# Performance work log

Hardware: AMD Instinct MI355X
Metric: run time of the kernel (lower is better)

The kernel has to match this reference:

```python
import jax, jax.numpy as jnp
import numpy as np

B, C, O, K, H, W = 32, 256, 256, 7, 31, 31


def _unfold(x, k):
    """Extract kxk sliding windows (stride 1, no padding, no dilation).

    x: [B, C, H, W] -> patches [B, C, k, k, Ho, Wo]
    """
    _, _, h, w = x.shape
    ho, wo = h - k + 1, w - k + 1
    # fixed small loop over k*k window offsets (k=7 -> 49 cheap slices)
    rows = []
    for i in range(k):
        cols = [x[:, :, i:i + ho, j:j + wo] for j in range(k)]
        rows.append(jnp.stack(cols, axis=2))  # [B, C, k, Ho, Wo]
    return jnp.stack(rows, axis=2)  # [B, C, k, k, Ho, Wo]


def setup_inputs() -> dict:
    key = jax.random.key(0)
    k1, k2, k3, k4 = jax.random.split(key, 4)
    x = jax.random.normal(k1, (B, C, H, W), dtype=jnp.float32)
    kernel = jax.random.normal(k2, (B, C, K, K), dtype=jnp.float32)
    weight = jax.random.normal(k3, (O, C, K, K), dtype=jnp.float32) * 0.02
    bias = jax.random.normal(k4, (O,), dtype=jnp.float32) * 0.02
    return {"x": x, "kernel": kernel, "weight": weight, "bias": bias}


def reference(x, kernel, weight, bias):
    k = weight.shape[-1]
    patches = _unfold(x, k)  # [B, C, k, k, Ho, Wo]
    # fused: (patches * kernel[..., None, None]) contracted with weight
    # torch: einsum('ijklmn,ojkl->iomn', patches * kernel_view, weight)
    out = jnp.einsum('bcklhw,bckl,ockl->bohw', patches, kernel, weight)
    out = out + bias[None, :, None, None]
    return out
```

## Files before the change

### kernel.cpp

```cpp
#include <hip/hip_runtime.h>
#include <hip/hip_bf16.h>

typedef __attribute__((ext_vector_type(8)))  short short8;
typedef __attribute__((ext_vector_type(4)))  float floatx4;
typedef __attribute__((ext_vector_type(16))) float floatx16;

#define BB 32
#define CC 256
#define OO 256
#define KS 7
#define HH 31
#define WW 31
#define HO 25
#define PP 625
#define SS 49

#define SLAB_PITCH 40
#define SLAB_ROWS  310

#define WT4_ELEMS  ((size_t)SS * 8 * 2 * CC * 16)
#define WT4_BYTES  (WT4_ELEMS * 2)
#define KERNF_BYTES ((size_t)BB * SS * CC * 4)
#define WMOD_ELEMS ((size_t)BB * WT4_ELEMS)
#define WMOD_BYTES (WMOD_ELEMS * 2)

static __device__ __forceinline__ unsigned pk2(float lo, float hi) {
    float2 f; f.x = lo; f.y = hi;
    __hip_bfloat162 h = __float22bfloat162_rn(f);
    unsigned r;
    __builtin_memcpy(&r, &h, sizeof(r));
    return r;
}
static __device__ __forceinline__ float bflo(unsigned u) {
    return __builtin_bit_cast(float, u << 16);
}
static __device__ __forceinline__ float bfhi(unsigned u) {
    return __builtin_bit_cast(float, u & 0xffff0000u);
}

static __device__ __forceinline__ uint4 modpack(uint4 wv, float4 k0, float4 k1) {
    float p0 = bflo(wv.x) * k0.x, p1 = bfhi(wv.x) * k0.y;
    float p2 = bflo(wv.y) * k0.z, p3 = bfhi(wv.y) * k0.w;
    float p4 = bflo(wv.z) * k1.x, p5 = bfhi(wv.z) * k1.y;
    float p6 = bflo(wv.w) * k1.z, p7 = bfhi(wv.w) * k1.w;
    uint4 r;
    r.x = pk2(p0, p1); r.y = pk2(p2, p3); r.z = pk2(p4, p5); r.w = pk2(p6, p7);
    return r;
}

__global__ __launch_bounds__(256) void repack_w(const float* __restrict__ w,
                                                unsigned short* __restrict__ wt4) {
    const int bid = blockIdx.x;
    const int s = bid >> 3, cb = bid & 7;
    const int o = threadIdx.x;
    const float* src = w + ((size_t)o * CC + cb * 32) * SS + s;
    float v[32];
#pragma unroll
    for (int ci = 0; ci < 32; ++ci) v[ci] = src[(size_t)ci * SS];
#pragma unroll
    for (int kh = 0; kh < 2; ++kh) {
        unsigned short* dst = wt4 + ((size_t)bid * 2 + kh) * (CC * 16) + o * 16;
        uint4 p0, p1;
        p0.x = pk2(v[kh*16+0], v[kh*16+1]);  p0.y = pk2(v[kh*16+2], v[kh*16+3]);
        p0.z = pk2(v[kh*16+4], v[kh*16+5]);  p0.w = pk2(v[kh*16+6], v[kh*16+7]);
        p1.x = pk2(v[kh*16+8], v[kh*16+9]);  p1.y = pk2(v[kh*16+10], v[kh*16+11]);
        p1.z = pk2(v[kh*16+12], v[kh*16+13]); p1.w = pk2(v[kh*16+14], v[kh*16+15]);
        *(uint4*)(dst)     = p0;
        *(uint4*)(dst + 8) = p1;
    }
}

__global__ __launch_bounds__(256) void repack_k(const float* __restrict__ kern,
                                                float* __restrict__ kernf) {
    const int bid = blockIdx.x;
    const int b = bid / KS, kk = bid % KS;
    const int c = threadIdx.x;
    const float* src = kern + ((size_t)b * CC + c) * SS + kk * KS;
#pragma unroll
    for (int ll = 0; ll < KS; ++ll)
        kernf[((size_t)b * SS + kk * KS + ll) * CC + c] = src[ll];
}

__global__ __launch_bounds__(256) void premod(
        const unsigned short* __restrict__ wt4, const float* __restrict__ kern,
        unsigned short* __restrict__ wmod) {
    const int bid = blockIdx.x;
    const int b = bid / 392, rc = bid % 392;
    const int s = rc >> 3, cb = rc & 7;
    const int o = threadIdx.x;
    const float* kp = kern + ((size_t)b * CC + cb * 32) * SS + s;
    float kf[32];
#pragma unroll
    for (int ci = 0; ci < 32; ++ci) kf[ci] = kp[(size_t)ci * SS];
#pragma unroll
    for (int kh = 0; kh < 2; ++kh) {
        const size_t off = ((size_t)rc * 2 + kh) * (CC * 16) + o * 16;
        uint4 w0 = *(const uint4*)(wt4 + off);
        uint4 w1 = *(const uint4*)(wt4 + off + 8);
        float4 k0a, k0b, k1a, k1b;
        k0a.x = kf[kh*16+0];  k0a.y = kf[kh*16+1];  k0a.z = kf[kh*16+2];  k0a.w = kf[kh*16+3];
        k0b.x = kf[kh*16+4];  k0b.y = kf[kh*16+5];  k0b.z = kf[kh*16+6];  k0b.w = kf[kh*16+7];
        k1a.x = kf[kh*16+8];  k1a.y = kf[kh*16+9];  k1a.z = kf[kh*16+10]; k1a.w = kf[kh*16+11];
        k1b.x = kf[kh*16+12]; k1b.y = kf[kh*16+13]; k1b.z = kf[kh*16+14]; k1b.w = kf[kh*16+15];
        uint4 m0 = modpack(w0, k0a, k0b);
        uint4 m1 = modpack(w1, k1a, k1b);
        unsigned short* dst = wmod + (size_t)b * WT4_ELEMS + off;
        *(uint4*)(dst)     = m0;
        *(uint4*)(dst + 8) = m1;
    }
}

__global__ __launch_bounds__(256, 4) void dwconv_big(
        const float* __restrict__ x, const unsigned short* __restrict__ wmod,
        const float* __restrict__ bias, float* __restrict__ out) {
    __shared__ unsigned short slab[SLAB_ROWS * SLAB_PITCH];

    const int tid = threadIdx.x;
    const int id = blockIdx.x;
    const int hi = id / 80, rem = id % 80;
    const int px = rem >> 3;
    const int g = hi * 8 + (rem & 7);
    const int b = g >> 2, oy = g & 3;

    const int p0 = px * 64, o0 = oy * 64;
    const int h0 = p0 / HO;
    const int pmax = (p0 + 63 < PP - 1) ? p0 + 63 : PP - 1;
    const int rows = pmax / HO - h0 + 7;
    const int npos = rows * WW;

    const int lane = tid & 63, kw = tid >> 6;
    const int l32 = lane & 31, half = lane >> 5;

    int bOff[2];
#pragma unroll
    for (int ph = 0; ph < 2; ++ph) {
        int p = p0 + ph * 32 + l32;
        if (p > PP - 1) p = PP - 1;
        int h = p / HO, ww_ = p - h * HO;
        bOff[ph] = ((h - h0) * WW + ww_) * SLAB_PITCH + half * 8;
    }

    const int s0 = kw * 12 + (kw > 0 ? 1 : 0);
    const int ns = kw ? 12 : 13;

    const unsigned short* wmodb = wmod + (size_t)b * WT4_ELEMS
                                  + (size_t)(o0 + l32) * 16 + half * 8;

    floatx16 acc[2][2];
#pragma unroll
    for (int oh = 0; oh < 2; ++oh)
#pragma unroll
        for (int ph = 0; ph < 2; ++ph)
#pragma unroll
            for (int r = 0; r < 16; ++r) acc[oh][ph][r] = 0.f;

    for (int cb = 0; cb < 8; ++cb) {
        __syncthreads();
        {
            const float* xsrc = x + ((size_t)(b * CC + cb * 32 + kw * 8)) * (HH * WW)
                                  + h0 * WW;
#pragma unroll
            for (int it = 0; it < 5; ++it) {
                int pos = lane + it * 64;
                if (pos < npos) {
                    float v[8];
#pragma unroll
                    for (int j = 0; j < 8; ++j) v[j] = xsrc[j * (HH * WW) + pos];
                    uint4 pkt;
                    pkt.x = pk2(v[0], v[1]); pkt.y = pk2(v[2], v[3]);
                    pkt.z = pk2(v[4], v[5]); pkt.w = pk2(v[6], v[7]);
                    *(uint4*)(slab + pos * SLAB_PITCH + kw * 8) = pkt;
                }
            }
        }
        __syncthreads();

        const unsigned short* aptr = wmodb + (size_t)(s0 * 8 + cb) * 8192;

        uint4 wa0 = *(const uint4*)(aptr);
        uint4 wa1 = *(const uint4*)(aptr + 512);
        uint4 wa2 = *(const uint4*)(aptr + 4096);
        uint4 wa3 = *(const uint4*)(aptr + 4096 + 512);

        int s = s0, kk = s0 / KS, ll = s0 - (s0 / KS) * KS;
        for (int si = 0; si < ns; ++si) {
            uint4 wn0, wn1, wn2, wn3;
            if (si + 1 < ns) {
                aptr += 65536;
                wn0 = *(const uint4*)(aptr);
                wn1 = *(const uint4*)(aptr + 512);
                wn2 = *(const uint4*)(aptr + 4096);
                wn3 = *(const uint4*)(aptr + 4096 + 512);
            } else {
                wn0 = wa0; wn1 = wa1; wn2 = wa2; wn3 = wa3;
            }

            const unsigned short* slabS = slab + (kk * WW + ll) * SLAB_PITCH;
            short8 sb00 = *(const short8*)(slabS + bOff[0]);
            short8 sb01 = *(const short8*)(slabS + bOff[0] + 16);
            short8 sb10 = *(const short8*)(slabS + bOff[1]);
            short8 sb11 = *(const short8*)(slabS + bOff[1] + 16);

            short8 a00 = __builtin_bit_cast(short8, wa0);
            short8 a10 = __builtin_bit_cast(short8, wa1);
            short8 a01 = __builtin_bit_cast(short8, wa2);
            short8 a11 = __builtin_bit_cast(short8, wa3);

            acc[0][0] = __builtin_amdgcn_mfma_f32_32x32x16_bf16(a00, sb00, acc[0][0], 0, 0, 0);
            acc[0][1] = __builtin_amdgcn_mfma_f32_32x32x16_bf16(a00, sb10, acc[0][1], 0, 0, 0);
            acc[1][0] = __builtin_amdgcn_mfma_f32_32x32x16_bf16(a10, sb00, acc[1][0], 0, 0, 0);
            acc[1][1] = __builtin_amdgcn_mfma_f32_32x32x16_bf16(a10, sb10, acc[1][1], 0, 0, 0);
            acc[0][0] = __builtin_amdgcn_mfma_f32_32x32x16_bf16(a01, sb01, acc[0][0], 0, 0, 0);
            acc[0][1] = __builtin_amdgcn_mfma_f32_32x32x16_bf16(a01, sb11, acc[0][1], 0, 0, 0);
            acc[1][0] = __builtin_amdgcn_mfma_f32_32x32x16_bf16(a11, sb01, acc[1][0], 0, 0, 0);
            acc[1][1] = __builtin_amdgcn_mfma_f32_32x32x16_bf16(a11, sb11, acc[1][1], 0, 0, 0);

            wa0 = wn0; wa1 = wn1; wa2 = wn2; wa3 = wn3;
            ++s; if (++ll == KS) { ll = 0; ++kk; }
        }
    }

    float* red = (float*)slab;
    __syncthreads();
    if (kw == 3) {
#pragma unroll
        for (int oh = 0; oh < 2; ++oh)
#pragma unroll
            for (int ph = 0; ph < 2; ++ph)
#pragma unroll
                for (int c = 0; c < 4; ++c) {
                    floatx4 v4 = {acc[oh][ph][4*c+0], acc[oh][ph][4*c+1],
                                  acc[oh][ph][4*c+2], acc[oh][ph][4*c+3]};
                    *(floatx4*)(red + (ph * 32 + l32) * 68 + oh * 32 + c * 8 + 4 * half) = v4;
                }
    }
    __syncthreads();
    if (kw == 2) {
#pragma unroll
        for (int oh = 0; oh < 2; ++oh)
#pragma unroll
            for (int ph = 0; ph < 2; ++ph)
#pragma unroll
                for (int c = 0; c < 4; ++c) {
                    float* rp = red + (ph * 32 + l32) * 68 + oh * 32 + c * 8 + 4 * half;
                    floatx4 v4 = *(floatx4*)rp;
                    v4[0] += acc[oh][ph][4*c+0]; v4[1] += acc[oh][ph][4*c+1];
                    v4[2] += acc[oh][ph][4*c+2]; v4[3] += acc[oh][ph][4*c+3];
                    *(floatx4*)rp = v4;
                }
    }
    __syncthreads();
    if (kw == 1) {
#pragma unroll
        for (int oh = 0; oh < 2; ++oh)
#pragma unroll
            for (int ph = 0; ph < 2; ++ph)
#pragma unroll
                for (int c = 0; c < 4; ++c) {
                    float* rp = red + (ph * 32 + l32) * 68 + oh * 32 + c * 8 + 4 * half;
                    floatx4 v4 = *(floatx4*)rp;
                    v4[0] += acc[oh][ph][4*c+0]; v4[1] += acc[oh][ph][4*c+1];
                    v4[2] += acc[oh][ph][4*c+2]; v4[3] += acc[oh][ph][4*c+3];
                    *(floatx4*)rp = v4;
                }
    }
    __syncthreads();
    if (kw == 0) {
#pragma unroll
        for (int oh = 0; oh < 2; ++oh)
#pragma unroll
            for (int c = 0; c < 4; ++c) {
                const int ob = o0 + oh * 32 + c * 8 + 4 * half;
                const float4 bv = *(const float4*)(bias + ob);
#pragma unroll
                for (int ph = 0; ph < 2; ++ph) {
                    const int p = p0 + ph * 32 + l32;
                    floatx4 v4 = *(floatx4*)(red + (ph * 32 + l32) * 68 + oh * 32 + c * 8 + 4 * half);
                    if (p < PP) {
                        out[((size_t)(b * OO + ob + 0)) * PP + p] = v4[0] + acc[oh][ph][4*c+0] + bv.x;
                        out[((size_t)(b * OO + ob + 1)) * PP + p] = v4[1] + acc[oh][ph][4*c+1] + bv.y;
                        out[((size_t)(b * OO + ob + 2)) * PP + p] = v4[2] + acc[oh][ph][4*c+2] + bv.z;
                        out[((size_t)(b * OO + ob + 3)) * PP + p] = v4[3] + acc[oh][ph][4*c+3] + bv.w;
                    }
                }
            }
    }
}

#define SLAB2_ROWS 372
__global__ __launch_bounds__(256, 3) void dwconv_mid(
        const float* __restrict__ x,
        const unsigned short* __restrict__ wt4, const float* __restrict__ kernf,
        const float* __restrict__ bias, float* __restrict__ out) {
    __shared__ unsigned short slab[SLAB2_ROWS * SLAB_PITCH];

    const int tid = threadIdx.x;
    const int id = blockIdx.x;
    const int oy = id & 3;
    const int t  = id >> 2;
    const int px = t % 5, b = t / 5;
    const int p0 = px * 128, o0 = oy * 64;
    const int h0 = p0 / HO;
    const int rows = (HH - h0) < 12 ? (HH - h0) : 12;
    const int npos = rows * WW;

    const int lane = tid & 63, wid = tid >> 6;
    const int pw = wid & 1, kw = wid >> 1;
    const int lo16 = lane & 15, quad = lane >> 4;

    int bOff[4];
#pragma unroll
    for (int pt = 0; pt < 4; ++pt) {
        int p = p0 + pw * 64 + pt * 16 + lo16;
        if (p > PP - 1) p = PP - 1;
        int h = p / HO, ww_ = p - h * HO;
        bOff[pt] = ((h - h0) * WW + ww_) * SLAB_PITCH + quad * 8;
    }

    const int s0 = kw ? 25 : 0;
    const int ns = kw ? 24 : 25;

    floatx4 acc[4][4];
#pragma unroll
    for (int at = 0; at < 4; ++at)
#pragma unroll
        for (int pt = 0; pt < 4; ++pt)
            acc[at][pt] = (floatx4){0.f, 0.f, 0.f, 0.f};

    for (int cb = 0; cb < 8; ++cb) {
        __syncthreads();
        {
            const int coct = wid;
            const float* xsrc = x + ((size_t)(b * CC + cb * 32 + coct * 8)) * (HH * WW)
                                  + h0 * WW;
#pragma unroll
            for (int it = 0; it < 6; ++it) {
                int pos = lane + it * 64;
                if (pos < npos) {
                    float v[8];
#pragma unroll
                    for (int j = 0; j < 8; ++j) v[j] = xsrc[j * (HH * WW) + pos];
                    uint4 pkt;
                    pkt.x = pk2(v[0], v[1]); pkt.y = pk2(v[2], v[3]);
                    pkt.z = pk2(v[4], v[5]); pkt.w = pk2(v[6], v[7]);
                    *(uint4*)(slab + pos * SLAB_PITCH + coct * 8) = pkt;
                }
            }
        }
        __syncthreads();

        const unsigned short* aptrA = wt4 +
            ((size_t)(s0 * 8 + cb) * 2 + (quad >> 1)) * 4096 +
            (size_t)(o0 + lo16) * 16 + (quad & 1) * 8;
        const float* kptr = kernf + ((size_t)b * SS + s0) * CC + cb * 32 + quad * 8;

        uint4 wa[4];
        wa[0] = *(const uint4*)(aptrA);
        wa[1] = *(const uint4*)(aptrA + 256);
        wa[2] = *(const uint4*)(aptrA + 512);
        wa[3] = *(const uint4*)(aptrA + 768);
        float4 kq0 = *(const float4*)(kptr);
        float4 kq1 = *(const float4*)(kptr + 4);

        for (int si = 0; si < ns; ++si) {
            const int s = s0 + si;
            uint4 wn[4]; float4 kn0, kn1;
            if (si + 1 < ns) {
                aptrA += 65536;
                kptr  += CC;
                wn[0] = *(const uint4*)(aptrA);
                wn[1] = *(const uint4*)(aptrA + 256);
                wn[2] = *(const uint4*)(aptrA + 512);
                wn[3] = *(const uint4*)(aptrA + 768);
                kn0 = *(const float4*)(kptr);
                kn1 = *(const float4*)(kptr + 4);
            } else {
                wn[0] = wa[0]; wn[1] = wa[1]; wn[2] = wa[2]; wn[3] = wa[3];
                kn0 = kq0; kn1 = kq1;
            }

            const int kk = s / KS, ll = s - kk * KS;
            const unsigned short* slabS = slab + (kk * WW + ll) * SLAB_PITCH;

            short8 sb0 = *(const short8*)(slabS + bOff[0]);
            short8 sb1 = *(const short8*)(slabS + bOff[1]);
            short8 sb2 = *(const short8*)(slabS + bOff[2]);
            short8 sb3 = *(const short8*)(slabS + bOff[3]);

            short8 sa0 = __builtin_bit_cast(short8, modpack(wa[0], kq0, kq1));
            short8 sa1 = __builtin_bit_cast(short8, modpack(wa[1], kq0, kq1));
            short8 sa2 = __builtin_bit_cast(short8, modpack(wa[2], kq0, kq1));
            short8 sa3 = __builtin_bit_cast(short8, modpack(wa[3], kq0, kq1));

            acc[0][0] = __builtin_amdgcn_mfma_f32_16x16x32_bf16(sa0, sb0, acc[0][0], 0, 0, 0);
            acc[0][1] = __builtin_amdgcn_mfma_f32_16x16x32_bf16(sa0, sb1, acc[0][1], 0, 0, 0);
            acc[0][2] = __builtin_amdgcn_mfma_f32_16x16x32_bf16(sa0, sb2, acc[0][2], 0, 0, 0);
            acc[0][3] = __builtin_amdgcn_mfma_f32_16x16x32_bf16(sa0, sb3, acc[0][3], 0, 0, 0);
            acc[1][0] = __builtin_amdgcn_mfma_f32_16x16x32_bf16(sa1, sb0, acc[1][0], 0, 0, 0);
            acc[1][1] = __builtin_amdgcn_mfma_f32_16x16x32_bf16(sa1, sb1, acc[1][1], 0, 0, 0);
            acc[1][2] = __builtin_amdgcn_mfma_f32_16x16x32_bf16(sa1, sb2, acc[1][2], 0, 0, 0);
            acc[1][3] = __builtin_amdgcn_mfma_f32_16x16x32_bf16(sa1, sb3, acc[1][3], 0, 0, 0);
            acc[2][0] = __builtin_amdgcn_mfma_f32_16x16x32_bf16(sa2, sb0, acc[2][0], 0, 0, 0);
            acc[2][1] = __builtin_amdgcn_mfma_f32_16x16x32_bf16(sa2, sb1, acc[2][1], 0, 0, 0);
            acc[2][2] = __builtin_amdgcn_mfma_f32_16x16x32_bf16(sa2, sb2, acc[2][2], 0, 0, 0);
            acc[2][3] = __builtin_amdgcn_mfma_f32_16x16x32_bf16(sa2, sb3, acc[2][3], 0, 0, 0);
            acc[3][0] = __builtin_amdgcn_mfma_f32_16x16x32_bf16(sa3, sb0, acc[3][0], 0, 0, 0);
            acc[3][1] = __builtin_amdgcn_mfma_f32_16x16x32_bf16(sa3, sb1, acc[3][1], 0, 0, 0);
            acc[3][2] = __builtin_amdgcn_mfma_f32_16x16x32_bf16(sa3, sb2, acc[3][2], 0, 0, 0);
            acc[3][3] = __builtin_amdgcn_mfma_f32_16x16x32_bf16(sa3, sb3, acc[3][3], 0, 0, 0);

            wa[0] = wn[0]; wa[1] = wn[1]; wa[2] = wn[2]; wa[3] = wn[3];
            kq0 = kn0; kq1 = kn1;
        }
    }

    float* red = (float*)slab;
    for (int round = 0; round < 2; ++round) {
        __syncthreads();
        if (kw == 1 && pw == round) {
#pragma unroll
            for (int at = 0; at < 4; ++at)
#pragma unroll
                for (int pt = 0; pt < 4; ++pt)
                    *(floatx4*)(red + (pt * 16 + lo16) * 68 + at * 16 + quad * 4)
                        = acc[at][pt];
        }
        __syncthreads();
        if (kw == 0 && pw == round) {
#pragma unroll
            for (int at = 0; at < 4; ++at) {
                const float4 bv = *(const float4*)(bias + o0 + at * 16 + quad * 4);
#pragma unroll
                for (int pt = 0; pt < 4; ++pt) {
                    floatx4 v = *(const floatx4*)(red + (pt * 16 + lo16) * 68
                                                  + at * 16 + quad * 4);
                    int p = p0 + round * 64 + pt * 16 + lo16;
                    if (p < PP) {
                        const int ob = o0 + at * 16 + quad * 4;
                        out[((size_t)(b * OO + ob + 0)) * PP + p] = acc[at][pt][0] + v[0] + bv.x;
                        out[((size_t)(b * OO + ob + 1)) * PP + p] = acc[at][pt][1] + v[1] + bv.y;
                        out[((size_t)(b * OO + ob + 2)) * PP + p] = acc[at][pt][2] + v[2] + bv.z;
                        out[((size_t)(b * OO + ob + 3)) * PP + p] = acc[at][pt][3] + v[3] + bv.w;
                    }
                }
            }
        }
    }
}

__global__ __launch_bounds__(256) void dwconv_naive(
        const float* __restrict__ x, const float* __restrict__ kern,
        const float* __restrict__ w, const float* __restrict__ bias,
        float* __restrict__ out) {
    const int idx = blockIdx.x * 256 + threadIdx.x;
    if (idx >= BB * OO * PP) return;
    const int p = idx % PP;
    const int o = (idx / PP) % OO;
    const int b = idx / (PP * OO);
    const int h = p / HO;
    const int wq = p - h * HO;
    float acc = 0.f;
    for (int c = 0; c < CC; ++c) {
        const float* xp = x + ((size_t)(b * CC + c)) * (HH * WW) + h * WW + wq;
        const float* kp = kern + ((size_t)b * CC + c) * SS;
        const float* wp = w + ((size_t)o * CC + c) * SS;
#pragma unroll
        for (int s = 0; s < SS; ++s) {
            const int kk = s / KS;
            const int ll = s - kk * KS;
            acc += xp[kk * WW + ll] * kp[s] * wp[s];
        }
    }
    out[idx] = acc + bias[o];
}

extern "C" void kernel_launch(void* const* d_in, const int* in_sizes, int n_in,
                              void* d_out, int out_size, void* d_ws, size_t ws_size,
                              hipStream_t stream) {
    const float* x    = (const float*)d_in[0];
    const float* kern = (const float*)d_in[1];
    const float* w    = (const float*)d_in[2];
    const float* bias = (const float*)d_in[3];
    float* out = (float*)d_out;

    if (ws_size >= WT4_BYTES + WMOD_BYTES) {
        unsigned short* wt4  = (unsigned short*)d_ws;
        unsigned short* wmod = (unsigned short*)((char*)d_ws + WT4_BYTES);
        repack_w<<<dim3(SS * 8), dim3(256), 0, stream>>>(w, wt4);
        premod<<<dim3(BB * SS * 8), dim3(256), 0, stream>>>(wt4, kern, wmod);
        dwconv_big<<<dim3(1280), dim3(256), 0, stream>>>(x, wmod, bias, out);
    } else if (ws_size >= WT4_BYTES + KERNF_BYTES) {
        unsigned short* wt4 = (unsigned short*)d_ws;
        float* kernf = (float*)((char*)d_ws + WT4_BYTES);
        repack_w<<<dim3(SS * 8), dim3(256), 0, stream>>>(w, wt4);
        repack_k<<<dim3(BB * KS), dim3(256), 0, stream>>>(kern, kernf);
        dwconv_mid<<<dim3(640), dim3(256), 0, stream>>>(x, wt4, kernf, bias, out);
    } else {
        const int total = BB * OO * PP;
        dwconv_naive<<<dim3((total + 255) / 256), dim3(256), 0, stream>>>(
            x, kern, w, bias, out);
    }
}
```

Measured before the change: 307.8 us.

## Double pixel tile per block in dwconv_big to reuse modulated weights

Measured after the change: 340.5 us. +10.6%, slower.

```diff
diff --git a/kernel.cpp b/kernel.cpp
--- a/kernel.cpp
+++ b/kernel.cpp
@@ -16,7 +16,7 @@
 #define SS 49
 
 #define SLAB_PITCH 40
-#define SLAB_ROWS  310
+#define SLAB_ROWS  372
 
 #define WT4_ELEMS  ((size_t)SS * 8 * 2 * CC * 16)
 #define WT4_BYTES  (WT4_ELEMS * 2)
@@ -110,30 +110,30 @@
     }
 }
 
-__global__ __launch_bounds__(256, 4) void dwconv_big(
+__global__ __launch_bounds__(256, 2) void dwconv_big(
         const float* __restrict__ x, const unsigned short* __restrict__ wmod,
         const float* __restrict__ bias, float* __restrict__ out) {
     __shared__ unsigned short slab[SLAB_ROWS * SLAB_PITCH];
 
     const int tid = threadIdx.x;
     const int id = blockIdx.x;
-    const int hi = id / 80, rem = id % 80;
+    const int hi = id / 40, rem = id % 40;
     const int px = rem >> 3;
     const int g = hi * 8 + (rem & 7);
     const int b = g >> 2, oy = g & 3;
 
-    const int p0 = px * 64, o0 = oy * 64;
+    const int p0 = px * 128, o0 = oy * 64;
     const int h0 = p0 / HO;
-    const int pmax = (p0 + 63 < PP - 1) ? p0 + 63 : PP - 1;
+    const int pmax = (p0 + 127 < PP - 1) ? p0 + 127 : PP - 1;
     const int rows = pmax / HO - h0 + 7;
     const int npos = rows * WW;
 
     const int lane = tid & 63, kw = tid >> 6;
     const int l32 = lane & 31, half = lane >> 5;
 
-    int bOff[2];
-#pragma unroll
-    for (int ph = 0; ph < 2; ++ph) {
+    int bOff[4];
+#pragma unroll
+    for (int ph = 0; ph < 4; ++ph) {
         int p = p0 + ph * 32 + l32;
         if (p > PP - 1) p = PP - 1;
         int h = p / HO, ww_ = p - h * HO;
@@ -146,11 +146,11 @@
     const unsigned short* wmodb = wmod + (size_t)b * WT4_ELEMS
                                   + (size_t)(o0 + l32) * 16 + half * 8;
 
-    floatx16 acc[2][2];
+    floatx16 acc[2][4];
 #pragma unroll
     for (int oh = 0; oh < 2; ++oh)
 #pragma unroll
-        for (int ph = 0; ph < 2; ++ph)
+        for (int ph = 0; ph < 4; ++ph)
 #pragma unroll
             for (int r = 0; r < 16; ++r) acc[oh][ph][r] = 0.f;
 
@@ -160,7 +160,7 @@
             const float* xsrc = x + ((size_t)(b * CC + cb * 32 + kw * 8)) * (HH * WW)
                                   + h0 * WW;
 #pragma unroll
-            for (int it = 0; it < 5; ++it) {
+            for (int it = 0; it < 6; ++it) {
                 int pos = lane + it * 64;
                 if (pos < npos) {
                     float v[8];
@@ -182,7 +182,7 @@
         uint4 wa2 = *(const uint4*)(aptr + 4096);
         uint4 wa3 = *(const uint4*)(aptr + 4096 + 512);
 
-        int s = s0, kk = s0 / KS, ll = s0 - (s0 / KS) * KS;
+        int kk = s0 / KS, ll = s0 - (s0 / KS) * KS;
         for (int si = 0; si < ns; ++si) {
             uint4 wn0, wn1, wn2, wn3;
             if (si + 1 < ns) {
@@ -196,103 +196,105 @@
             }
 
             const unsigned short* slabS = slab + (kk * WW + ll) * SLAB_PITCH;
-            short8 sb00 = *(const short8*)(slabS + bOff[0]);
-            short8 sb01 = *(const short8*)(slabS + bOff[0] + 16);
-            short8 sb10 = *(const short8*)(slabS + bOff[1]);
-            short8 sb11 = *(const short8*)(slabS + bOff[1] + 16);
-
             short8 a00 = __builtin_bit_cast(short8, wa0);
             short8 a10 = __builtin_bit_cast(short8, wa1);
             short8 a01 = __builtin_bit_cast(short8, wa2);
             short8 a11 = __builtin_bit_cast(short8, wa3);
 
-            acc[0][0] = __builtin_amdgcn_mfma_f32_32x32x16_bf16(a00, sb00, acc[0][0], 0, 0, 0);
-            acc[0][1] = __builtin_amdgcn_mfma_f32_32x32x16_bf16(a00, sb10, acc[0][1], 0, 0, 0);
-            acc[1][0] = __builtin_amdgcn_mfma_f32_32x32x16_bf16(a10, sb00, acc[1][0], 0, 0, 0);
-            acc[1][1] = __builtin_amdgcn_mfma_f32_32x32x16_bf16(a10, sb10, acc[1][1], 0, 0, 0);
-            acc[0][0] = __builtin_amdgcn_mfma_f32_32x32x16_bf16(a01, sb01, acc[0][0], 0, 0, 0);
-            acc[0][1] = __builtin_amdgcn_mfma_f32_32x32x16_bf16(a01, sb11, acc[0][1], 0, 0, 0);
-            acc[1][0] = __builtin_amdgcn_mfma_f32_32x32x16_bf16(a11, sb01, acc[1][0], 0, 0, 0);
-            acc[1][1] = __builtin_amdgcn_mfma_f32_32x32x16_bf16(a11, sb11, acc[1][1], 0, 0, 0);
+#pragma unroll
+            for (int ph = 0; ph < 4; ++ph) {
+                short8 sbk0 = *(const short8*)(slabS + bOff[ph]);
+                short8 sbk1 = *(const short8*)(slabS + bOff[ph] + 16);
+                acc[0][ph] = __builtin_amdgcn_mfma_f32_32x32x16_bf16(a00, sbk0, acc[0][ph], 0, 0, 0);
+                acc[1][ph] = __builtin_amdgcn_mfma_f32_32x32x16_bf16(a10, sbk0, acc[1][ph], 0, 0, 0);
+                acc[0][ph] = __builtin_amdgcn_mfma_f32_32x32x16_bf16(a01, sbk1, acc[0][ph], 0, 0, 0);
+                acc[1][ph] = __builtin_amdgcn_mfma_f32_32x32x16_bf16(a11, sbk1, acc[1][ph], 0, 0, 0);
+            }
 
             wa0 = wn0; wa1 = wn1; wa2 = wn2; wa3 = wn3;
-            ++s; if (++ll == KS) { ll = 0; ++kk; }
+            if (++ll == KS) { ll = 0; ++kk; }
         }
     }
 
     float* red = (float*)slab;
-    __syncthreads();
-    if (kw == 3) {
-#pragma unroll
-        for (int oh = 0; oh < 2; ++oh)
-#pragma unroll
-            for (int ph = 0; ph < 2; ++ph)
+#pragma unroll
+    for (int round = 0; round < 2; ++round) {
+        __syncthreads();
+        if (kw == 3) {
+#pragma unroll
+            for (int oh = 0; oh < 2; ++oh)
+#pragma unroll
+                for (int phl = 0; phl < 2; ++phl)
+#pragma unroll
+                    for (int c = 0; c < 4; ++c) {
+                        const int ph = round * 2 + phl;
+                        floatx4 v4 = {acc[oh][ph][4*c+0], acc[oh][ph][4*c+1],
+                                      acc[oh][ph][4*c+2], acc[oh][ph][4*c+3]};
+                        *(floatx4*)(red + (phl * 32 + l32) * 68 + oh * 32 + c * 8 + 4 * half) = v4;
+                    }
+        }
+        __syncthreads();
+        if (kw == 2) {
+#pragma unroll
+            for (int oh = 0; oh < 2; ++oh)
+#pragma unroll
+                for (int phl = 0; phl < 2; ++phl)
+#pragma unroll
+                    for (int c = 0; c < 4; ++c) {
+                        const int ph = round * 2 + phl;
+                        float* rp = red + (phl * 32 + l32) * 68 + oh * 32 + c * 8 + 4 * half;
+                        floatx4 v4 = *(floatx4*)rp;
+                        v4[0] += acc[oh][ph][4*c+0]; v4[1] += acc[oh][ph][4*c+1];
+                        v4[2] += acc[oh][ph][4*c+2]; v4[3] += acc[oh][ph][4*c+3];
+                        *(floatx4*)rp = v4;
+                    }
+        }
+        __syncthreads();
+        if (kw == 1) {
+#pragma unroll
+            for (int oh = 0; oh < 2; ++oh)
+#pragma unroll
+                for (int phl = 0; phl < 2; ++phl)
+#pragma unroll
+                    for (int c = 0; c < 4; ++c) {
+                        const int ph = round * 2 + phl;
+                        float* rp = red + (phl * 32 + l32) * 68 + oh * 32 + c * 8 + 4 * half;
+                        floatx4 v4 = *(floatx4*)rp;
+                        v4[0] += acc[oh][ph][4*c+0]; v4[1] += acc[oh][ph][4*c+1];
+                        v4[2] += acc[oh][ph][4*c+2]; v4[3] += acc[oh][ph][4*c+3];
+                        *(floatx4*)rp = v4;
+                    }
+        }
+        __syncthreads();
+        if (kw == 0) {
+#pragma unroll
+            for (int oh = 0; oh < 2; ++oh)
 #pragma unroll
                 for (int c = 0; c < 4; ++c) {
-                    floatx4 v4 = {acc[oh][ph][4*c+0], acc[oh][ph][4*c+1],
-                                  acc[oh][ph][4*c+2], acc[oh][ph][4*c+3]};
-                    *(floatx4*)(red + (ph * 32 + l32) * 68 + oh * 32 + c * 8 + 4 * half) = v4;
-                }
-    }
-    __syncthreads();
-    if (kw == 2) {
-#pragma unroll
-        for (int oh = 0; oh < 2; ++oh)
-#pragma unroll
-            for (int ph = 0; ph < 2; ++ph)
-#pragma unroll
-                for (int c = 0; c < 4; ++c) {
-                    float* rp = red + (ph * 32 + l32) * 68 + oh * 32 + c * 8 + 4 * half;
-                    floatx4 v4 = *(floatx4*)rp;
-                    v4[0] += acc[oh][ph][4*c+0]; v4[1] += acc[oh][ph][4*c+1];
-                    v4[2] += acc[oh][ph][4*c+2]; v4[3] += acc[oh][ph][4*c+3];
-                    *(floatx4*)rp = v4;
-                }
-    }
-    __syncthreads();
-    if (kw == 1) {
-#pragma unroll
-        for (int oh = 0; oh < 2; ++oh)
-#pragma unroll
-            for (int ph = 0; ph < 2; ++ph)
-#pragma unroll
-                for (int c = 0; c < 4; ++c) {
-                    float* rp = red + (ph * 32 + l32) * 68 + oh * 32 + c * 8 + 4 * half;
-                    floatx4 v4 = *(floatx4*)rp;
-                    v4[0] += acc[oh][ph][4*c+0]; v4[1] += acc[oh][ph][4*c+1];
-                    v4[2] += acc[oh][ph][4*c+2]; v4[3] += acc[oh][ph][4*c+3];
-                    *(floatx4*)rp = v4;
-                }
-    }
-    __syncthreads();
-    if (kw == 0) {
-#pragma unroll
-        for (int oh = 0; oh < 2; ++oh)
-#pragma unroll
-            for (int c = 0; c < 4; ++c) {
-                const int ob = o0 + oh * 32 + c * 8 + 4 * half;
-                const float4 bv = *(const float4*)(bias + ob);
-#pragma unroll
-                for (int ph = 0; ph < 2; ++ph) {
-                    const int p = p0 + ph * 32 + l32;
-                    floatx4 v4 = *(floatx4*)(red + (ph * 32 + l32) * 68 + oh * 32 + c * 8 + 4 * half);
-                    if (p < PP) {
-                        out[((size_t)(b * OO + ob + 0)) * PP + p] = v4[0] + acc[oh][ph][4*c+0] + bv.x;
-                        out[((size_t)(b * OO + ob + 1)) * PP + p] = v4[1] + acc[oh][ph][4*c+1] + bv.y;
-                        out[((size_t)(b * OO + ob + 2)) * PP + p] = v4[2] + acc[oh][ph][4*c+2] + bv.z;
-                        out[((size_t)(b * OO + ob + 3)) * PP + p] = v4[3] + acc[oh][ph][4*c+3] + bv.w;
+                    const int ob = o0 + oh * 32 + c * 8 + 4 * half;
+                    const float4 bv = *(const float4*)(bias + ob);
+#pragma unroll
+                    for (int phl = 0; phl < 2; ++phl) {
+                        const int ph = round * 2 + phl;
+                        const int p = p0 + ph * 32 + l32;
+                        floatx4 v4 = *(floatx4*)(red + (phl * 32 + l32) * 68 + oh * 32 + c * 8 + 4 * half);
+                        if (p < PP) {
+                            out[((size_t)(b * OO + ob + 0)) * PP + p] = v4[0] + acc[oh][ph][4*c+0] + bv.x;
+                            out[((size_t)(b * OO + ob + 1)) * PP + p] = v4[1] + acc[oh][ph][4*c+1] + bv.y;
+                            out[((size_t)(b * OO + ob + 2)) * PP + p] = v4[2] + acc[oh][ph][4*c+2] + bv.z;
+                            out[((size_t)(b * OO + ob + 3)) * PP + p] = v4[3] + acc[oh][ph][4*c+3] + bv.w;
+                        }
                     }
                 }
-            }
-    }
-}
-
-#define SLAB2_ROWS 372
+        }
+    }
+}
+
 __global__ __launch_bounds__(256, 3) void dwconv_mid(
         const float* __restrict__ x,
         const unsigned short* __restrict__ wt4, const float* __restrict__ kernf,
         const float* __restrict__ bias, float* __restrict__ out) {
-    __shared__ unsigned short slab[SLAB2_ROWS * SLAB_PITCH];
+    __shared__ unsigned short slab[SLAB_ROWS * SLAB_PITCH];
 
     const int tid = threadIdx.x;
     const int id = blockIdx.x;
@@ -488,7 +490,7 @@
         unsigned short* wmod = (unsigned short*)((char*)d_ws + WT4_BYTES);
         repack_w<<<dim3(SS * 8), dim3(256), 0, stream>>>(w, wt4);
         premod<<<dim3(BB * SS * 8), dim3(256), 0, stream>>>(wt4, kern, wmod);
-        dwconv_big<<<dim3(1280), dim3(256), 0, stream>>>(x, wmod, bias, out);
+        dwconv_big<<<dim3(640), dim3(256), 0, stream>>>(x, wmod, bias, out);
     } else if (ws_size >= WT4_BYTES + KERNF_BYTES) {
         unsigned short* wt4 = (unsigned short*)d_ws;
         float* kernf = (float*)((char*)d_ws + WT4_BYTES);
```

## Pre-convert x to padded bf16 slabs and load them into LDS directly

Applied to the files above, without the earlier changes.

Result: slower. 351.2 us (+14.1%).

```diff
diff --git a/kernel.cpp b/kernel.cpp
--- a/kernel.cpp
+++ b/kernel.cpp
@@ -15,14 +15,17 @@
 #define PP 625
 #define SS 49
 
-#define SLAB_PITCH 40
-#define SLAB_ROWS  310
+#define PITCH 40
 
 #define WT4_ELEMS  ((size_t)SS * 8 * 2 * CC * 16)
 #define WT4_BYTES  (WT4_ELEMS * 2)
 #define KERNF_BYTES ((size_t)BB * SS * CC * 4)
 #define WMOD_ELEMS ((size_t)BB * WT4_ELEMS)
 #define WMOD_BYTES (WMOD_ELEMS * 2)
+
+#define XSLICE_E   38440
+#define XSLICE_B   76880
+#define XBF_BYTES  ((size_t)BB * 8 * XSLICE_B + 2048)
 
 static __device__ __forceinline__ unsigned pk2(float lo, float hi) {
     float2 f; f.x = lo; f.y = hi;
@@ -36,6 +39,12 @@
 }
 static __device__ __forceinline__ float bfhi(unsigned u) {
     return __builtin_bit_cast(float, u & 0xffff0000u);
+}
+
+static __device__ __forceinline__ void gload_lds16(const void* g, void* l) {
+    __builtin_amdgcn_global_load_lds(
+        (const __attribute__((address_space(1))) unsigned int*)g,
+        (__attribute__((address_space(3))) unsigned int*)l, 16, 0, 0);
 }
 
 static __device__ __forceinline__ uint4 modpack(uint4 wv, float4 k0, float4 k1) {
@@ -110,10 +119,23 @@
     }
 }
 
-__global__ __launch_bounds__(256, 4) void dwconv_big(
-        const float* __restrict__ x, const unsigned short* __restrict__ wmod,
+__global__ __launch_bounds__(256) void xbf_prep(const float* __restrict__ x,
+                                                unsigned short* __restrict__ xbf) {
+    const int bid = blockIdx.x;
+    const int b = bid >> 3, cb = bid & 7;
+    const int ci = threadIdx.x & 31, pg = threadIdx.x >> 5;
+    const float* src = x + ((size_t)(b * CC + cb * 32 + ci)) * (HH * WW);
+    unsigned short* dst = xbf + (size_t)bid * XSLICE_E + ci;
+    for (int pos = pg; pos < HH * WW; pos += 8)
+        dst[pos * PITCH] = (unsigned short)(pk2(src[pos], 0.f) & 0xffffu);
+}
+
+__global__ __launch_bounds__(256, 4) void dwconv_bigx(
+        const unsigned short* __restrict__ xbf,
+        const unsigned short* __restrict__ wmod,
         const float* __restrict__ bias, float* __restrict__ out) {
-    __shared__ unsigned short slab[SLAB_ROWS * SLAB_PITCH];
+    __shared__ uint4 slabq[1600];
+    unsigned short* slab = (unsigned short*)slabq;
 
     const int tid = threadIdx.x;
     const int id = blockIdx.x;
@@ -127,6 +149,7 @@
     const int pmax = (p0 + 63 < PP - 1) ? p0 + 63 : PP - 1;
     const int rows = pmax / HO - h0 + 7;
     const int npos = rows * WW;
+    const int nch = (npos * 80 + 1023) >> 10;
 
     const int lane = tid & 63, kw = tid >> 6;
     const int l32 = lane & 31, half = lane >> 5;
@@ -137,7 +160,7 @@
         int p = p0 + ph * 32 + l32;
         if (p > PP - 1) p = PP - 1;
         int h = p / HO, ww_ = p - h * HO;
-        bOff[ph] = ((h - h0) * WW + ww_) * SLAB_PITCH + half * 8;
+        bOff[ph] = ((h - h0) * WW + ww_) * PITCH + half * 8;
     }
 
     const int s0 = kw * 12 + (kw > 0 ? 1 : 0);
@@ -145,6 +168,8 @@
 
     const unsigned short* wmodb = wmod + (size_t)b * WT4_ELEMS
                                   + (size_t)(o0 + l32) * 16 + half * 8;
+    const char* gslab = (const char*)xbf + (size_t)(b * 8) * XSLICE_B
+                        + (size_t)h0 * (WW * PITCH * 2) + lane * 16;
 
     floatx16 acc[2][2];
 #pragma unroll
@@ -157,32 +182,20 @@
     for (int cb = 0; cb < 8; ++cb) {
         __syncthreads();
         {
-            const float* xsrc = x + ((size_t)(b * CC + cb * 32 + kw * 8)) * (HH * WW)
-                                  + h0 * WW;
-#pragma unroll
-            for (int it = 0; it < 5; ++it) {
-                int pos = lane + it * 64;
-                if (pos < npos) {
-                    float v[8];
-#pragma unroll
-                    for (int j = 0; j < 8; ++j) v[j] = xsrc[j * (HH * WW) + pos];
-                    uint4 pkt;
-                    pkt.x = pk2(v[0], v[1]); pkt.y = pk2(v[2], v[3]);
-                    pkt.z = pk2(v[4], v[5]); pkt.w = pk2(v[6], v[7]);
-                    *(uint4*)(slab + pos * SLAB_PITCH + kw * 8) = pkt;
-                }
-            }
+            const char* gsrc = gslab + (size_t)cb * XSLICE_B;
+            char* lb = (char*)slab;
+            for (int c = kw; c < nch; c += 4)
+                gload_lds16(gsrc + c * 1024, lb + c * 1024);
         }
         __syncthreads();
 
         const unsigned short* aptr = wmodb + (size_t)(s0 * 8 + cb) * 8192;
-
         uint4 wa0 = *(const uint4*)(aptr);
         uint4 wa1 = *(const uint4*)(aptr + 512);
         uint4 wa2 = *(const uint4*)(aptr + 4096);
         uint4 wa3 = *(const uint4*)(aptr + 4096 + 512);
 
-        int s = s0, kk = s0 / KS, ll = s0 - (s0 / KS) * KS;
+        int kk = s0 / KS, ll = s0 - (s0 / KS) * KS;
         for (int si = 0; si < ns; ++si) {
             uint4 wn0, wn1, wn2, wn3;
             if (si + 1 < ns) {
@@ -195,7 +208,7 @@
                 wn0 = wa0; wn1 = wa1; wn2 = wa2; wn3 = wa3;
             }
 
-            const unsigned short* slabS = slab + (kk * WW + ll) * SLAB_PITCH;
+            const unsigned short* slabS = slab + (kk * WW + ll) * PITCH;
             short8 sb00 = *(const short8*)(slabS + bOff[0]);
             short8 sb01 = *(const short8*)(slabS + bOff[0] + 16);
             short8 sb10 = *(const short8*)(slabS + bOff[1]);
@@ -216,7 +229,7 @@
             acc[1][1] = __builtin_amdgcn_mfma_f32_32x32x16_bf16(a11, sb11, acc[1][1], 0, 0, 0);
 
             wa0 = wn0; wa1 = wn1; wa2 = wn2; wa3 = wn3;
-            ++s; if (++ll == KS) { ll = 0; ++kk; }
+            if (++ll == KS) { ll = 0; ++kk; }
         }
     }
 
@@ -287,12 +300,187 @@
     }
 }
 
-#define SLAB2_ROWS 372
+__global__ __launch_bounds__(256, 4) void dwconv_big7(
+        const float* __restrict__ x, const unsigned short* __restrict__ wmod,
+        const float* __restrict__ bias, float* __restrict__ out) {
+    __shared__ unsigned short slab[310 * PITCH];
+
+    const int tid = threadIdx.x;
+    const int id = blockIdx.x;
+    const int hi = id / 80, rem = id % 80;
+    const int px = rem >> 3;
+    const int g = hi * 8 + (rem & 7);
+    const int b = g >> 2, oy = g & 3;
+
+    const int p0 = px * 64, o0 = oy * 64;
+    const int h0 = p0 / HO;
+    const int pmax = (p0 + 63 < PP - 1) ? p0 + 63 : PP - 1;
+    const int rows = pmax / HO - h0 + 7;
+    const int npos = rows * WW;
+
+    const int lane = tid & 63, kw = tid >> 6;
+    const int l32 = lane & 31, half = lane >> 5;
+
+    int bOff[2];
+#pragma unroll
+    for (int ph = 0; ph < 2; ++ph) {
+        int p = p0 + ph * 32 + l32;
+        if (p > PP - 1) p = PP - 1;
+        int h = p / HO, ww_ = p - h * HO;
+        bOff[ph] = ((h - h0) * WW + ww_) * PITCH + half * 8;
+    }
+
+    const int s0 = kw * 12 + (kw > 0 ? 1 : 0);
+    const int ns = kw ? 12 : 13;
+
+    const unsigned short* wmodb = wmod + (size_t)b * WT4_ELEMS
+                                  + (size_t)(o0 + l32) * 16 + half * 8;
+
+    floatx16 acc[2][2];
+#pragma unroll
+    for (int oh = 0; oh < 2; ++oh)
+#pragma unroll
+        for (int ph = 0; ph < 2; ++ph)
+#pragma unroll
+            for (int r = 0; r < 16; ++r) acc[oh][ph][r] = 0.f;
+
+    for (int cb = 0; cb < 8; ++cb) {
+        __syncthreads();
+        {
+            const float* xsrc = x + ((size_t)(b * CC + cb * 32 + kw * 8)) * (HH * WW)
+                                  + h0 * WW;
+#pragma unroll
+            for (int it = 0; it < 5; ++it) {
+                int pos = lane + it * 64;
+                if (pos < npos) {
+                    float v[8];
+#pragma unroll
+                    for (int j = 0; j < 8; ++j) v[j] = xsrc[j * (HH * WW) + pos];
+                    uint4 pkt;
+                    pkt.x = pk2(v[0], v[1]); pkt.y = pk2(v[2], v[3]);
+                    pkt.z = pk2(v[4], v[5]); pkt.w = pk2(v[6], v[7]);
+                    *(uint4*)(slab + pos * PITCH + kw * 8) = pkt;
+                }
+            }
+        }
+        __syncthreads();
+
+        const unsigned short* aptr = wmodb + (size_t)(s0 * 8 + cb) * 8192;
+        uint4 wa0 = *(const uint4*)(aptr);
+        uint4 wa1 = *(const uint4*)(aptr + 512);
+        uint4 wa2 = *(const uint4*)(aptr + 4096);
+        uint4 wa3 = *(const uint4*)(aptr + 4096 + 512);
+
+        int kk = s0 / KS, ll = s0 - (s0 / KS) * KS;
+        for (int si = 0; si < ns; ++si) {
+            uint4 wn0, wn1, wn2, wn3;
+            if (si + 1 < ns) {
+                aptr += 65536;
+                wn0 = *(const uint4*)(aptr);
+                wn1 = *(const uint4*)(aptr + 512);
+                wn2 = *(const uint4*)(aptr + 4096);
+                wn3 = *(const uint4*)(aptr + 4096 + 512);
+            } else {
+                wn0 = wa0; wn1 = wa1; wn2 = wa2; wn3 = wa3;
+            }
+
+            const unsigned short* slabS = slab + (kk * WW + ll) * PITCH;
+            short8 sb00 = *(const short8*)(slabS + bOff[0]);
+            short8 sb01 = *(const short8*)(slabS + bOff[0] + 16);
+            short8 sb10 = *(const short8*)(slabS + bOff[1]);
+            short8 sb11 = *(const short8*)(slabS + bOff[1] + 16);
+
+            short8 a00 = __builtin_bit_cast(short8, wa0);
+            short8 a10 = __builtin_bit_cast(short8, wa1);
+            short8 a01 = __builtin_bit_cast(short8, wa2);
+            short8 a11 = __builtin_bit_cast(short8, wa3);
+
+            acc[0][0] = __builtin_amdgcn_mfma_f32_32x32x16_bf16(a00, sb00, acc[0][0], 0, 0, 0);
+            acc[0][1] = __builtin_amdgcn_mfma_f32_32x32x16_bf16(a00, sb10, acc[0][1], 0, 0, 0);
+            acc[1][0] = __builtin_amdgcn_mfma_f32_32x32x16_bf16(a10, sb00, acc[1][0], 0, 0, 0);
+            acc[1][1] = __builtin_amdgcn_mfma_f32_32x32x16_bf16(a10, sb10, acc[1][1], 0, 0, 0);
+            acc[0][0] = __builtin_amdgcn_mfma_f32_32x32x16_bf16(a01, sb01, acc[0][0], 0, 0, 0);
+            acc[0][1] = __builtin_amdgcn_mfma_f32_32x32x16_bf16(a01, sb11, acc[0][1], 0, 0, 0);
+            acc[1][0] = __builtin_amdgcn_mfma_f32_32x32x16_bf16(a11, sb01, acc[1][0], 0, 0, 0);
+            acc[1][1] = __builtin_amdgcn_mfma_f32_32x32x16_bf16(a11, sb11, acc[1][1], 0, 0, 0);
+
+            wa0 = wn0; wa1 = wn1; wa2 = wn2; wa3 = wn3;
+            if (++ll == KS) { ll = 0; ++kk; }
+        }
+    }
+
+    float* red = (float*)slab;
+    __syncthreads();
+    if (kw == 3) {
+#pragma unroll
+        for (int oh = 0; oh < 2; ++oh)
+#pragma unroll
+            for (int ph = 0; ph < 2; ++ph)
+#pragma unroll
+                for (int c = 0; c < 4; ++c) {
+                    floatx4 v4 = {acc[oh][ph][4*c+0], acc[oh][ph][4*c+1],
+                                  acc[oh][ph][4*c+2], acc[oh][ph][4*c+3]};
+                    *(floatx4*)(red + (ph * 32 + l32) * 68 + oh * 32 + c * 8 + 4 * half) = v4;
+                }
+    }
+    __syncthreads();
+    if (kw == 2) {
+#pragma unroll
+        for (int oh = 0; oh < 2; ++oh)
+#pragma unroll
+            for (int ph = 0; ph < 2; ++ph)
+#pragma unroll
+                for (int c = 0; c < 4; ++c) {
+                    float* rp = red + (ph * 32 + l32) * 68 + oh * 32 + c * 8 + 4 * half;
+                    floatx4 v4 = *(floatx4*)rp;
+                    v4[0] += acc[oh][ph][4*c+0]; v4[1] += acc[oh][ph][4*c+1];
+                    v4[2] += acc[oh][ph][4*c+2]; v4[3] += acc[oh][ph][4*c+3];
+                    *(floatx4*)rp = v4;
+                }
+    }
+    __syncthreads();
+    if (kw == 1) {
+#pragma unroll
+        for (int oh = 0; oh < 2; ++oh)
+#pragma unroll
+            for (int ph = 0; ph < 2; ++ph)
+#pragma unroll
+                for (int c = 0; c < 4; ++c) {
+                    float* rp = red + (ph * 32 + l32) * 68 + oh * 32 + c * 8 + 4 * half;
+                    floatx4 v4 = *(floatx4*)rp;
+                    v4[0] += acc[oh][ph][4*c+0]; v4[1] += acc[oh][ph][4*c+1];
+                    v4[2] += acc[oh][ph][4*c+2]; v4[3] += acc[oh][ph][4*c+3];
+                    *(floatx4*)rp = v4;
+                }
+    }
+    __syncthreads();
+    if (kw == 0) {
+#pragma unroll
+        for (int oh = 0; oh < 2; ++oh)
+#pragma unroll
+            for (int c = 0; c < 4; ++c) {
+                const int ob = o0 + oh * 32 + c * 8 + 4 * half;
+                const float4 bv = *(const float4*)(bias + ob);
+#pragma unroll
+                for (int ph = 0; ph < 2; ++ph) {
+                    const int p = p0 + ph * 32 + l32;
+                    floatx4 v4 = *(floatx4*)(red + (ph * 32 + l32) * 68 + oh * 32 + c * 8 + 4 * half);
+                    if (p < PP) {
+                        out[((size_t)(b * OO + ob + 0)) * PP + p] = v4[0] + acc[oh][ph][4*c+0] + bv.x;
+                        out[((size_t)(b * OO + ob + 1)) * PP + p] = v4[1] + acc[oh][ph][4*c+1] + bv.y;
+                        out[((size_t)(b * OO + ob + 2)) * PP + p] = v4[2] + acc[oh][ph][4*c+2] + bv.z;
+                        out[((size_t)(b * OO + ob + 3)) * PP + p] = v4[3] + acc[oh][ph][4*c+3] + bv.w;
+                    }
+                }
+            }
+    }
+}
+
 __global__ __launch_bounds__(256, 3) void dwconv_mid(
         const float* __restrict__ x,
         const unsigned short* __restrict__ wt4, const float* __restrict__ kernf,
         const float* __restrict__ bias, float* __restrict__ out) {
-    __shared__ unsigned short slab[SLAB2_ROWS * SLAB_PITCH];
+    __shared__ unsigned short slab[372 * PITCH];
 
     const int tid = threadIdx.x;
     const int id = blockIdx.x;
@@ -314,7 +502,7 @@
         int p = p0 + pw * 64 + pt * 16 + lo16;
         if (p > PP - 1) p = PP - 1;
         int h = p / HO, ww_ = p - h * HO;
-        bOff[pt] = ((h - h0) * WW + ww_) * SLAB_PITCH + quad * 8;
+        bOff[pt] = ((h - h0) * WW + ww_) * PITCH + quad * 8;
     }
 
     const int s0 = kw ? 25 : 0;
@@ -343,7 +531,7 @@
                     uint4 pkt;
                     pkt.x = pk2(v[0], v[1]); pkt.y = pk2(v[2], v[3]);
                     pkt.z = pk2(v[4], v[5]); pkt.w = pk2(v[6], v[7]);
-                    *(uint4*)(slab + pos * SLAB_PITCH + coct * 8) = pkt;
+                    *(uint4*)(slab + pos * PITCH + coct * 8) = pkt;
                 }
             }
         }
@@ -380,7 +568,7 @@
             }
 
             const int kk = s / KS, ll = s - kk * KS;
-            const unsigned short* slabS = slab + (kk * WW + ll) * SLAB_PITCH;
+            const unsigned short* slabS = slab + (kk * WW + ll) * PITCH;
 
             short8 sb0 = *(const short8*)(slabS + bOff[0]);
             short8 sb1 = *(const short8*)(slabS + bOff[1]);
@@ -483,12 +671,20 @@
     const float* bias = (const float*)d_in[3];
     float* out = (float*)d_out;
 
-    if (ws_size >= WT4_BYTES + WMOD_BYTES) {
+    if (ws_size >= WMOD_BYTES + XBF_BYTES) {
+        unsigned short* wmod = (unsigned short*)d_ws;
+        unsigned short* xbf  = (unsigned short*)((char*)d_ws + WMOD_BYTES);
+        unsigned short* wt4  = xbf;
+        repack_w<<<dim3(SS * 8), dim3(256), 0, stream>>>(w, wt4);
+        premod<<<dim3(BB * SS * 8), dim3(256), 0, stream>>>(wt4, kern, wmod);
+        xbf_prep<<<dim3(BB * 8), dim3(256), 0, stream>>>(x, xbf);
+        dwconv_bigx<<<dim3(1280), dim3(256), 0, stream>>>(xbf, wmod, bias, out);
+    } else if (ws_size >= WT4_BYTES + WMOD_BYTES) {
         unsigned short* wt4  = (unsigned short*)d_ws;
         unsigned short* wmod = (unsigned short*)((char*)d_ws + WT4_BYTES);
         repack_w<<<dim3(SS * 8), dim3(256), 0, stream>>>(w, wt4);
         premod<<<dim3(BB * SS * 8), dim3(256), 0, stream>>>(wt4, kern, wmod);
-        dwconv_big<<<dim3(1280), dim3(256), 0, stream>>>(x, wmod, bias, out);
+        dwconv_big7<<<dim3(1280), dim3(256), 0, stream>>>(x, wmod, bias, out);
     } else if (ws_size >= WT4_BYTES + KERNF_BYTES) {
         unsigned short* wt4 = (unsigned short*)d_ws;
         float* kernf = (float*)((char*)d_ws + WT4_BYTES);
```
